# Performance work log

Hardware: AMD Instinct MI355X
Metric: run time of the kernel (lower is better)

The kernel has to match this reference:

```python
import jax, jax.numpy as jnp
import numpy as np

B, S, E = 2, 2048, 2048
H, KV, D = 16, 4, 128
G = H // KV
ROPE_THETA = 10000.0


def setup_inputs() -> dict:
    key = jax.random.key(0)
    ks = jax.random.split(key, 8)
    std = 0.02
    return {
        "x": jax.random.normal(ks[0], (B, S, E), jnp.float32),
        "Wq": jax.random.normal(ks[1], (H * D, E), jnp.float32) * std,
        "bq": jax.random.normal(ks[2], (H * D,), jnp.float32) * std,
        "Wk": jax.random.normal(ks[3], (KV * D, E), jnp.float32) * std,
        "bk": jax.random.normal(ks[4], (KV * D,), jnp.float32) * std,
        "Wv": jax.random.normal(ks[5], (KV * D, E), jnp.float32) * std,
        "bv": jax.random.normal(ks[6], (KV * D,), jnp.float32) * std,
        "Wo": jax.random.normal(ks[7], (E, H * D), jnp.float32) * std,
    }


def _rope_cos_sin(seq_len, head_dim):
    inv_freq = 1.0 / (ROPE_THETA ** (jnp.arange(0, head_dim, 2, dtype=jnp.float32) / head_dim))
    pos = jnp.arange(seq_len, dtype=jnp.float32)  # rope scale factor = 1.0
    freqs = pos[:, None] * inv_freq[None, :]        # [S, D/2]
    emb = jnp.concatenate([freqs, freqs], axis=-1)  # [S, D]
    return jnp.cos(emb), jnp.sin(emb)


def _apply_rope(t, cos, sin):
    # t: [..., S, <extra dims>, D]; cos/sin: [S, D] broadcast over extra dims
    half = t.shape[-1] // 2
    extra = t.ndim - 3  # dims between S (axis 1) and D (last)
    c = cos.reshape((1, cos.shape[0]) + (1,) * extra + (cos.shape[1],))
    s = sin.reshape((1, sin.shape[0]) + (1,) * extra + (sin.shape[1],))
    rot = jnp.concatenate([-t[..., half:], t[..., :half]], axis=-1)
    return t * c + rot * s


def reference(x, Wq, bq, Wk, bk, Wv, bv, Wo):
    b, s, e = x.shape
    # QKV projections (biases on q/k/v, none on o)
    q = (jnp.einsum("bse,he->bsh", x, Wq) + bq).reshape(b, s, KV, G, D)
    k = (jnp.einsum("bse,he->bsh", x, Wk) + bk).reshape(b, s, KV, D)
    v = (jnp.einsum("bse,he->bsh", x, Wv) + bv).reshape(b, s, KV, D)

    cos, sin = _rope_cos_sin(s, D)
    q = _apply_rope(q, cos, sin)
    k = _apply_rope(k, cos, sin)

    scale = 1.0 / jnp.sqrt(jnp.float32(D))
    # GQA: q heads grouped per kv head; k/v broadcast over group dim
    scores = jnp.einsum("bskgd,btkd->bkgst", q, k) * scale  # [B,KV,G,S,S]
    causal = jnp.tril(jnp.ones((s, s), dtype=bool))
    scores = jnp.where(causal, scores, jnp.float32(-1e9))
    attn = jax.nn.softmax(scores, axis=-1)
    out = jnp.einsum("bkgst,btkd->bskgd", attn, v).reshape(b, s, H * D)
    return jnp.einsum("bsh,eh->bse", out, Wo)
```

## Files before the change

### kernel.cpp

```cpp
#include <hip/hip_runtime.h>
#include <hip/hip_bf16.h>
#include <math.h>

#define BB 2
#define SS 2048
#define EE 2048
#define HH 16
#define KVH 4
#define DD 128
#define QTILES 32

typedef short short8 __attribute__((ext_vector_type(8)));
typedef float f32x4 __attribute__((ext_vector_type(4)));

__device__ __forceinline__ unsigned int f2bf1(float x) {
    union { float f; unsigned int u; } v; v.f = x;
    return (v.u + 0x7FFFu + ((v.u >> 16) & 1u)) >> 16;
}
__device__ __forceinline__ unsigned int packbf(float a, float b) {
    return f2bf1(a) | (f2bf1(b) << 16);
}
__device__ __forceinline__ float bf2f(unsigned short u) {
    union { unsigned int u; float f; } v; v.u = ((unsigned int)u) << 16;
    return v.f;
}
__device__ __forceinline__ void gl_lds16(const void* g, void* l) {
    __builtin_amdgcn_global_load_lds(
        (const __attribute__((address_space(1))) unsigned int*)g,
        (__attribute__((address_space(3))) unsigned int*)l,
        16, 0, 0);
}

__global__ __launch_bounds__(256) void cvt_bf16_kernel(
    const float* __restrict__ in, unsigned short* __restrict__ out, int n4)
{
    int i = blockIdx.x * 256 + threadIdx.x;
    if (i < n4) {
        float4 f = ((const float4*)in)[i];
        ((uint2*)out)[i] = make_uint2(packbf(f.x, f.y), packbf(f.z, f.w));
    }
}

__global__ __launch_bounds__(256) void concat_bias_kernel(
    const float* __restrict__ bk, const float* __restrict__ bv, float* __restrict__ bkv)
{
    int i = blockIdx.x * 256 + threadIdx.x;
    bkv[i] = (i < 512) ? bk[i] : bv[i - 512];
}

template <bool OUT_BF16>
__global__ __launch_bounds__(256) void gemm_mfma_kernel(
    const unsigned short* __restrict__ A, const unsigned short* __restrict__ W,
    const float* __restrict__ bias, void* __restrict__ Cout,
    int M, int N, int K)
{
    __shared__ unsigned short As[128 * 32];
    __shared__ unsigned short Bs[128 * 32];

    const int tid  = threadIdx.x;
    const int w    = tid >> 6;
    const int lane = tid & 63;
    const int quad = lane >> 4;
    const int l16  = lane & 15;
    const int wr   = w >> 1, wc = w & 1;
    const int m0 = blockIdx.y * 128, n0 = blockIdx.x * 128;

    f32x4 acc[4][4];
#pragma unroll
    for (int i = 0; i < 4; ++i)
#pragma unroll
        for (int j = 0; j < 4; ++j) acc[i][j] = (f32x4){0.f, 0.f, 0.f, 0.f};

    const unsigned short* Ag = A + (size_t)(m0 + w * 32 + (lane >> 2)) * K + (lane & 3) * 8;
    const unsigned short* Wg = W + (size_t)(n0 + w * 32 + (lane >> 2)) * K + (lane & 3) * 8;
    unsigned short* AsB = &As[(w * 32) * 32];
    unsigned short* BsB = &Bs[(w * 32) * 32];

    for (int k0 = 0; k0 < K; k0 += 32) {
        gl_lds16(Ag + k0, AsB);
        gl_lds16(Ag + k0 + (size_t)16 * K, AsB + 16 * 32);
        gl_lds16(Wg + k0, BsB);
        gl_lds16(Wg + k0 + (size_t)16 * K, BsB + 16 * 32);
        __syncthreads();

        short8 a_f[4], b_f[4];
#pragma unroll
        for (int i = 0; i < 4; ++i)
            a_f[i] = *(const short8*)&As[(wr * 64 + i * 16 + l16) * 32 + quad * 8];
#pragma unroll
        for (int j = 0; j < 4; ++j)
            b_f[j] = *(const short8*)&Bs[(wc * 64 + j * 16 + l16) * 32 + quad * 8];
#pragma unroll
        for (int i = 0; i < 4; ++i)
#pragma unroll
            for (int j = 0; j < 4; ++j)
                acc[i][j] = __builtin_amdgcn_mfma_f32_16x16x32_bf16(a_f[i], b_f[j], acc[i][j], 0, 0, 0);
        __syncthreads();
    }

    float bj[4];
#pragma unroll
    for (int j = 0; j < 4; ++j)
        bj[j] = bias ? bias[n0 + wc * 64 + j * 16 + l16] : 0.0f;
#pragma unroll
    for (int i = 0; i < 4; ++i) {
#pragma unroll
        for (int r = 0; r < 4; ++r) {
            size_t row = m0 + wr * 64 + i * 16 + quad * 4 + r;
#pragma unroll
            for (int j = 0; j < 4; ++j) {
                size_t col = n0 + wc * 64 + j * 16 + l16;
                float val = acc[i][j][r] + bj[j];
                if (OUT_BF16)
                    ((unsigned short*)Cout)[row * N + col] = (unsigned short)f2bf1(val);
                else
                    ((float*)Cout)[row * N + col] = val;
            }
        }
    }
}

__global__ __launch_bounds__(64) void rope_bf16_kernel(
    unsigned short* __restrict__ t, int nh, int rowstride)
{
    int m = blockIdx.x / nh;
    int h = blockIdx.x % nh;
    int s = m % SS;
    int d = threadIdx.x;
    unsigned short* p = t + (size_t)m * rowstride + h * 128;
    float inv_freq = expf(-(float)d * (logf(10000.0f) / 64.0f));
    float fr = (float)s * inv_freq;
    float c = cosf(fr), sn = sinf(fr);
    float x1 = bf2f(p[d]), x2 = bf2f(p[d + 64]);
    p[d]      = (unsigned short)f2bf1(x1 * c - x2 * sn);
    p[d + 64] = (unsigned short)f2bf1(x2 * c + x1 * sn);
}

__global__ __launch_bounds__(256, 2) void attn_mfma_kernel(
    const unsigned short* __restrict__ q, const unsigned short* __restrict__ kvb,
    unsigned short* __restrict__ o)
{
    __shared__ unsigned int Ks_u[64 * 68];
    __shared__ unsigned int Vs_u[128 * 36];
    __shared__ short Ps[4][16 * 72];

    const int tid  = threadIdx.x;
    const int w    = tid >> 6;
    const int lane = tid & 63;
    const int quad = lane >> 4;
    const int l16  = lane & 15;
    const int jpair = blockIdx.x;
    const int h     = blockIdx.y;
    const int b     = blockIdx.z;
    const int kv    = h >> 2;

    const float scale = 0.08838834764831845f;
    const unsigned short* kbase = kvb + (size_t)b * SS * 1024 + kv * 128;
    const unsigned short* vbase = kbase + 512;

    for (int pass = 0; pass < 2; ++pass) {
        const int qt = pass ? (QTILES - 1 - jpair) : jpair;
        const int q0 = qt * 64;

        short8 qf[4];
        {
            const int sq = q0 + w * 16 + l16;
            const unsigned short* qp = q + (size_t)(b * SS + sq) * 2048 + h * 128 + quad * 8;
#pragma unroll
            for (int ks = 0; ks < 4; ++ks)
                qf[ks] = *(const short8*)(qp + ks * 32);
        }

        float m_r[4], l_r[4];
        f32x4 Oacc[8];
#pragma unroll
        for (int r = 0; r < 4; ++r) { m_r[r] = -1e30f; l_r[r] = 0.0f; }
#pragma unroll
        for (int ot = 0; ot < 8; ++ot) Oacc[ot] = (f32x4){0.f, 0.f, 0.f, 0.f};

        for (int t = 0; t <= qt; ++t) {
            const int p0 = t * 64;

            {
                const int c  = tid & 15;
                const int pb = tid >> 4;
#pragma unroll
                for (int rr = 0; rr < 4; ++rr) {
                    int pos = pb + rr * 16;
                    *(uint4*)(&Ks_u[pos * 68 + c * 4]) =
                        *(const uint4*)(kbase + (size_t)(p0 + pos) * 1024 + c * 8);
                }
            }
            {
                const int pp   = tid >> 3;
                const int dseg = (tid & 7) * 16;
                const unsigned short* va = vbase + (size_t)(p0 + 2 * pp) * 1024 + dseg;
                uint4 ua0 = *(const uint4*)(va);
                uint4 ua1 = *(const uint4*)(va + 8);
                uint4 ub0 = *(const uint4*)(va + 1024);
                uint4 ub1 = *(const uint4*)(va + 1024 + 8);
#define WR2(i, a, bb2) { \
    Vs_u[(dseg + (i)) * 36 + pp]     = ((a) & 0xffffu) | ((bb2) << 16); \
    Vs_u[(dseg + (i) + 1) * 36 + pp] = ((a) >> 16) | ((bb2) & 0xffff0000u); }
                WR2(0,  ua0.x, ub0.x) WR2(2,  ua0.y, ub0.y)
                WR2(4,  ua0.z, ub0.z) WR2(6,  ua0.w, ub0.w)
                WR2(8,  ua1.x, ub1.x) WR2(10, ua1.y, ub1.y)
                WR2(12, ua1.z, ub1.z) WR2(14, ua1.w, ub1.w)
#undef WR2
            }
            __syncthreads();

            f32x4 S[4];
#pragma unroll
            for (int ct = 0; ct < 4; ++ct) {
                f32x4 s = (f32x4){0.f, 0.f, 0.f, 0.f};
#pragma unroll
                for (int ks = 0; ks < 4; ++ks) {
                    short8 kf = *(const short8*)(&Ks_u[(ct * 16 + l16) * 68 + ks * 16 + quad * 4]);
                    s = __builtin_amdgcn_mfma_f32_16x16x32_bf16(qf[ks], kf, s, 0, 0, 0);
                }
#pragma unroll
                for (int r = 0; r < 4; ++r) s[r] *= scale;
                S[ct] = s;
            }

            if (t == qt) {
                const int rowloc = w * 16 + quad * 4;
#pragma unroll
                for (int ct = 0; ct < 4; ++ct)
#pragma unroll
                    for (int r = 0; r < 4; ++r)
                        if (ct * 16 + l16 > rowloc + r) S[ct][r] = -1e30f;
            }

            float mnew[4];
#pragma unroll
            for (int r = 0; r < 4; ++r) {
                float c0 = fmaxf(fmaxf(S[0][r], S[1][r]), fmaxf(S[2][r], S[3][r]));
                c0 = fmaxf(c0, __shfl_xor(c0, 1));
                c0 = fmaxf(c0, __shfl_xor(c0, 2));
                c0 = fmaxf(c0, __shfl_xor(c0, 4));
                c0 = fmaxf(c0, __shfl_xor(c0, 8));
                mnew[r] = fmaxf(m_r[r], c0);
            }
#pragma unroll
            for (int r = 0; r < 4; ++r) {
                float alpha = __expf(m_r[r] - mnew[r]);
                m_r[r] = mnew[r];
                float rs = 0.0f;
#pragma unroll
                for (int ct = 0; ct < 4; ++ct) {
                    float p = __expf(S[ct][r] - mnew[r]);
                    rs += p;
                    Ps[w][(quad * 4 + r) * 72 + ct * 16 + l16] = (short)f2bf1(p);
                }
                rs += __shfl_xor(rs, 1);
                rs += __shfl_xor(rs, 2);
                rs += __shfl_xor(rs, 4);
                rs += __shfl_xor(rs, 8);
                l_r[r] = l_r[r] * alpha + rs;
#pragma unroll
                for (int ot = 0; ot < 8; ++ot) Oacc[ot][r] *= alpha;
            }

            short8 pf0 = *(const short8*)(&Ps[w][l16 * 72 + quad * 8]);
            short8 pf1 = *(const short8*)(&Ps[w][l16 * 72 + 32 + quad * 8]);
#pragma unroll
            for (int ot = 0; ot < 8; ++ot) {
                short8 b0 = *(const short8*)((const short*)&Vs_u[(ot * 16 + l16) * 36 + quad * 4]);
                Oacc[ot] = __builtin_amdgcn_mfma_f32_16x16x32_bf16(pf0, b0, Oacc[ot], 0, 0, 0);
                short8 b1 = *(const short8*)((const short*)&Vs_u[(ot * 16 + l16) * 36 + 16 + quad * 4]);
                Oacc[ot] = __builtin_amdgcn_mfma_f32_16x16x32_bf16(pf1, b1, Oacc[ot], 0, 0, 0);
            }
            __syncthreads();
        }

        float inv[4];
#pragma unroll
        for (int r = 0; r < 4; ++r) inv[r] = 1.0f / l_r[r];
        const int orow0 = q0 + w * 16 + quad * 4;
        unsigned short* ob = o + (size_t)(b * SS + orow0) * 2048 + h * 128 + l16;
#pragma unroll
        for (int r = 0; r < 4; ++r)
#pragma unroll
            for (int ot = 0; ot < 8; ++ot)
                ob[(size_t)r * 2048 + ot * 16] = (unsigned short)f2bf1(Oacc[ot][r] * inv[r]);
    }
}

extern "C" void kernel_launch(void* const* d_in, const int* in_sizes, int n_in,
                              void* d_out, int out_size, void* d_ws, size_t ws_size,
                              hipStream_t stream)
{
    const float* x  = (const float*)d_in[0];
    const float* Wq = (const float*)d_in[1];
    const float* bq = (const float*)d_in[2];
    const float* Wk = (const float*)d_in[3];
    const float* bk = (const float*)d_in[4];
    const float* Wv = (const float*)d_in[5];
    const float* bv = (const float*)d_in[6];
    const float* Wo = (const float*)d_in[7];
    float* out = (float*)d_out;

    const int M = BB * SS;
    char* wsb = (char*)d_ws;
    unsigned short* xb   = (unsigned short*)wsb;  wsb += (size_t)M * EE * 2;
    unsigned short* wqb  = (unsigned short*)wsb;  wsb += (size_t)EE * EE * 2;
    unsigned short* wkvb = (unsigned short*)wsb;  wsb += (size_t)1024 * EE * 2;
    unsigned short* wob  = (unsigned short*)wsb;  wsb += (size_t)EE * EE * 2;
    unsigned short* qb   = (unsigned short*)wsb;  wsb += (size_t)M * 2048 * 2;
    unsigned short* kvb  = (unsigned short*)wsb;  wsb += (size_t)M * 1024 * 2;
    unsigned short* abb  = (unsigned short*)wsb;  wsb += (size_t)M * 2048 * 2;
    float* bkv = (float*)wsb;

    cvt_bf16_kernel<<<(M * EE / 4) / 256, 256, 0, stream>>>(x, xb, M * EE / 4);
    cvt_bf16_kernel<<<(EE * EE / 4) / 256, 256, 0, stream>>>(Wq, wqb, EE * EE / 4);
    cvt_bf16_kernel<<<(512 * EE / 4) / 256, 256, 0, stream>>>(Wk, wkvb, 512 * EE / 4);
    cvt_bf16_kernel<<<(512 * EE / 4) / 256, 256, 0, stream>>>(Wv, wkvb + (size_t)512 * EE, 512 * EE / 4);
    cvt_bf16_kernel<<<(EE * EE / 4) / 256, 256, 0, stream>>>(Wo, wob, EE * EE / 4);
    concat_bias_kernel<<<4, 256, 0, stream>>>(bk, bv, bkv);

    gemm_mfma_kernel<true><<<dim3(2048 / 128, M / 128), 256, 0, stream>>>(
        xb, wqb, bq, qb, M, 2048, EE);
    gemm_mfma_kernel<true><<<dim3(1024 / 128, M / 128), 256, 0, stream>>>(
        xb, wkvb, bkv, kvb, M, 1024, EE);

    rope_bf16_kernel<<<M * HH, 64, 0, stream>>>(qb, HH, 2048);
    rope_bf16_kernel<<<M * KVH, 64, 0, stream>>>(kvb, KVH, 1024);

    attn_mfma_kernel<<<dim3(16, HH, BB), 256, 0, stream>>>(qb, kvb, abb);

    gemm_mfma_kernel<false><<<dim3(EE / 128, M / 128), 256, 0, stream>>>(
        abb, wob, nullptr, out, M, EE, 2048);
}
```

Measured before the change: 421.3 us.

## Fuse QKV projection, merge prep kernels, double-buffer and swizzle attention LDS

Merges all fp32-to-bf16 conversions and the bias concatenation into one launch, fuses the Q and KV projections into a single GEMM over a combined QKV buffer, and merges the two RoPE launches. In the attention kernel, K/V tiles are prefetched into registers and stored into double-buffered LDS with XOR swizzles instead of padding, which removes one barrier per tile. Softmax now uses exp2 with the scale folded in. This cuts launch overhead and LDS bank conflicts at the cost of more registers and more complex indexing.

```diff
diff --git a/kernel.cpp b/kernel.cpp
--- a/kernel.cpp
+++ b/kernel.cpp
@@ -20,10 +20,6 @@
 __device__ __forceinline__ unsigned int packbf(float a, float b) {
     return f2bf1(a) | (f2bf1(b) << 16);
 }
-__device__ __forceinline__ float bf2f(unsigned short u) {
-    union { unsigned int u; float f; } v; v.u = ((unsigned int)u) << 16;
-    return v.f;
-}
 __device__ __forceinline__ void gl_lds16(const void* g, void* l) {
     __builtin_amdgcn_global_load_lds(
         (const __attribute__((address_space(1))) unsigned int*)g,
@@ -31,21 +27,32 @@
         16, 0, 0);
 }
 
-__global__ __launch_bounds__(256) void cvt_bf16_kernel(
-    const float* __restrict__ in, unsigned short* __restrict__ out, int n4)
-{
-    int i = blockIdx.x * 256 + threadIdx.x;
-    if (i < n4) {
-        float4 f = ((const float4*)in)[i];
-        ((uint2*)out)[i] = make_uint2(packbf(f.x, f.y), packbf(f.z, f.w));
-    }
-}
-
-__global__ __launch_bounds__(256) void concat_bias_kernel(
-    const float* __restrict__ bk, const float* __restrict__ bv, float* __restrict__ bkv)
-{
-    int i = blockIdx.x * 256 + threadIdx.x;
-    bkv[i] = (i < 512) ? bk[i] : bv[i - 512];
+__global__ __launch_bounds__(256) void cvt_all_kernel(
+    const float* __restrict__ x,  const float* __restrict__ Wq,
+    const float* __restrict__ Wk, const float* __restrict__ Wv,
+    const float* __restrict__ Wo, const float* __restrict__ bq,
+    const float* __restrict__ bk, const float* __restrict__ bv,
+    unsigned short* __restrict__ xb, unsigned short* __restrict__ wqkv,
+    unsigned short* __restrict__ wob, float* __restrict__ bqkv)
+{
+    long id = (long)blockIdx.x * 256 + threadIdx.x;
+    const float* src; unsigned short* dst; long j;
+    if (id < 2097152)      { j = id;           src = x;  dst = xb; }
+    else if (id < 3145728) { j = id - 2097152; src = Wq; dst = wqkv; }
+    else if (id < 3407872) { j = id - 3145728; src = Wk; dst = wqkv + 4194304; }
+    else if (id < 3670016) { j = id - 3407872; src = Wv; dst = wqkv + 5242880; }
+    else if (id < 4718592) { j = id - 3670016; src = Wo; dst = wob; }
+    else if (id < 4719360) {
+        long c = (id - 4718592) * 4;
+#pragma unroll
+        for (int e = 0; e < 4; ++e) {
+            long cc = c + e;
+            bqkv[cc] = (cc < 2048) ? bq[cc] : (cc < 2560 ? bk[cc - 2048] : bv[cc - 2560]);
+        }
+        return;
+    } else return;
+    float4 f = ((const float4*)src)[j];
+    ((uint2*)dst)[j] = make_uint2(packbf(f.x, f.y), packbf(f.z, f.w));
 }
 
 template <bool OUT_BF16>
@@ -120,29 +127,31 @@
     }
 }
 
-__global__ __launch_bounds__(64) void rope_bf16_kernel(
-    unsigned short* __restrict__ t, int nh, int rowstride)
-{
-    int m = blockIdx.x / nh;
-    int h = blockIdx.x % nh;
-    int s = m % SS;
+__global__ __launch_bounds__(64) void rope_kernel(unsigned short* __restrict__ qkv)
+{
+    int bix = blockIdx.x;
+    int m, col;
+    if (bix < 65536) { m = bix >> 4; col = (bix & 15) * 128; }
+    else { int i = bix - 65536; m = i >> 2; col = 2048 + (i & 3) * 128; }
+    int s = m & (SS - 1);
     int d = threadIdx.x;
-    unsigned short* p = t + (size_t)m * rowstride + h * 128;
+    unsigned short* p = qkv + (size_t)m * 3072 + col;
     float inv_freq = expf(-(float)d * (logf(10000.0f) / 64.0f));
     float fr = (float)s * inv_freq;
     float c = cosf(fr), sn = sinf(fr);
-    float x1 = bf2f(p[d]), x2 = bf2f(p[d + 64]);
-    p[d]      = (unsigned short)f2bf1(x1 * c - x2 * sn);
-    p[d + 64] = (unsigned short)f2bf1(x2 * c + x1 * sn);
+    union { unsigned int u; float f; } x1, x2;
+    x1.u = ((unsigned int)p[d]) << 16;
+    x2.u = ((unsigned int)p[d + 64]) << 16;
+    p[d]      = (unsigned short)f2bf1(x1.f * c - x2.f * sn);
+    p[d + 64] = (unsigned short)f2bf1(x2.f * c + x1.f * sn);
 }
 
 __global__ __launch_bounds__(256, 2) void attn_mfma_kernel(
-    const unsigned short* __restrict__ q, const unsigned short* __restrict__ kvb,
-    unsigned short* __restrict__ o)
-{
-    __shared__ unsigned int Ks_u[64 * 68];
-    __shared__ unsigned int Vs_u[128 * 36];
-    __shared__ short Ps[4][16 * 72];
+    const unsigned short* __restrict__ qkv, unsigned short* __restrict__ o)
+{
+    __shared__ unsigned int Ks_u[2][64 * 64];
+    __shared__ unsigned int Vs_u[2][128 * 32];
+    __shared__ unsigned short Ps[4][16 * 64];
 
     const int tid  = threadIdx.x;
     const int w    = tid >> 6;
@@ -154,9 +163,15 @@
     const int b     = blockIdx.z;
     const int kv    = h >> 2;
 
-    const float scale = 0.08838834764831845f;
-    const unsigned short* kbase = kvb + (size_t)b * SS * 1024 + kv * 128;
+    const float k2 = 0.12752789744920764f;
+
+    const unsigned short* kbase = qkv + (size_t)b * SS * 3072 + 2048 + kv * 128;
     const unsigned short* vbase = kbase + 512;
+
+    const int kc  = tid & 15;
+    const int kp0 = tid >> 4;
+    const int vpp = tid >> 3;
+    const int vd0 = (tid & 7) * 16;
 
     for (int pass = 0; pass < 2; ++pass) {
         const int qt = pass ? (QTILES - 1 - jpair) : jpair;
@@ -164,13 +179,25 @@
 
         short8 qf[4];
         {
-            const int sq = q0 + w * 16 + l16;
-            const unsigned short* qp = q + (size_t)(b * SS + sq) * 2048 + h * 128 + quad * 8;
+            const unsigned short* qp = qkv + (size_t)(b * SS + q0 + w * 16 + l16) * 3072 + h * 128 + quad * 8;
 #pragma unroll
             for (int ks = 0; ks < 4; ++ks)
                 qf[ks] = *(const short8*)(qp + ks * 32);
         }
 
+        uint4 kpre[4], vpa[2], vpb[2];
+        {
+            const unsigned short* kg = kbase + (size_t)kp0 * 3072 + kc * 8;
+#pragma unroll
+            for (int rr = 0; rr < 4; ++rr)
+                kpre[rr] = *(const uint4*)(kg + (size_t)rr * 16 * 3072);
+            const unsigned short* vg = vbase + (size_t)(2 * vpp) * 3072 + vd0;
+            vpa[0] = *(const uint4*)(vg);
+            vpa[1] = *(const uint4*)(vg + 8);
+            vpb[0] = *(const uint4*)(vg + 3072);
+            vpb[1] = *(const uint4*)(vg + 3072 + 8);
+        }
+
         float m_r[4], l_r[4];
         f32x4 Oacc[8];
 #pragma unroll
@@ -179,34 +206,42 @@
         for (int ot = 0; ot < 8; ++ot) Oacc[ot] = (f32x4){0.f, 0.f, 0.f, 0.f};
 
         for (int t = 0; t <= qt; ++t) {
-            const int p0 = t * 64;
-
+            const int buf = t & 1;
+            unsigned int* Kb = Ks_u[buf];
+            unsigned int* Vb = Vs_u[buf];
+
+#pragma unroll
+            for (int rr = 0; rr < 4; ++rr) {
+                int pos = kp0 + rr * 16;
+                int key = (kp0 + rr) & 7;
+                *(uint4*)&Kb[pos * 64 + (kc ^ key) * 4] = kpre[rr];
+            }
             {
-                const int c  = tid & 15;
-                const int pb = tid >> 4;
-#pragma unroll
-                for (int rr = 0; rr < 4; ++rr) {
-                    int pos = pb + rr * 16;
-                    *(uint4*)(&Ks_u[pos * 68 + c * 4]) =
-                        *(const uint4*)(kbase + (size_t)(p0 + pos) * 1024 + c * 8);
+                const unsigned int* pa = (const unsigned int*)vpa;
+                const unsigned int* pb = (const unsigned int*)vpb;
+#pragma unroll
+                for (int j = 0; j < 8; ++j) {
+                    unsigned lo = __builtin_amdgcn_perm(pb[j], pa[j], 0x05040100);
+                    unsigned hi = __builtin_amdgcn_perm(pb[j], pa[j], 0x07060302);
+                    int d0 = vd0 + 2 * j;
+                    int g  = d0 >> 4;
+                    int k0 = (d0 + g) & 7;
+                    int k1 = (d0 + 1 + g) & 7;
+                    Vb[d0 * 32 + (((vpp >> 2) ^ k0) & 7) * 4 + (vpp & 3)] = lo;
+                    Vb[(d0 + 1) * 32 + (((vpp >> 2) ^ k1) & 7) * 4 + (vpp & 3)] = hi;
                 }
             }
-            {
-                const int pp   = tid >> 3;
-                const int dseg = (tid & 7) * 16;
-                const unsigned short* va = vbase + (size_t)(p0 + 2 * pp) * 1024 + dseg;
-                uint4 ua0 = *(const uint4*)(va);
-                uint4 ua1 = *(const uint4*)(va + 8);
-                uint4 ub0 = *(const uint4*)(va + 1024);
-                uint4 ub1 = *(const uint4*)(va + 1024 + 8);
-#define WR2(i, a, bb2) { \
-    Vs_u[(dseg + (i)) * 36 + pp]     = ((a) & 0xffffu) | ((bb2) << 16); \
-    Vs_u[(dseg + (i) + 1) * 36 + pp] = ((a) >> 16) | ((bb2) & 0xffff0000u); }
-                WR2(0,  ua0.x, ub0.x) WR2(2,  ua0.y, ub0.y)
-                WR2(4,  ua0.z, ub0.z) WR2(6,  ua0.w, ub0.w)
-                WR2(8,  ua1.x, ub1.x) WR2(10, ua1.y, ub1.y)
-                WR2(12, ua1.z, ub1.z) WR2(14, ua1.w, ub1.w)
-#undef WR2
+
+            if (t < qt) {
+                const unsigned short* kg = kbase + (size_t)((t + 1) * 64 + kp0) * 3072 + kc * 8;
+#pragma unroll
+                for (int rr = 0; rr < 4; ++rr)
+                    kpre[rr] = *(const uint4*)(kg + (size_t)rr * 16 * 3072);
+                const unsigned short* vg = vbase + (size_t)((t + 1) * 64 + 2 * vpp) * 3072 + vd0;
+                vpa[0] = *(const uint4*)(vg);
+                vpa[1] = *(const uint4*)(vg + 8);
+                vpb[0] = *(const uint4*)(vg + 3072);
+                vpb[1] = *(const uint4*)(vg + 3072 + 8);
             }
             __syncthreads();
 
@@ -214,13 +249,13 @@
 #pragma unroll
             for (int ct = 0; ct < 4; ++ct) {
                 f32x4 s = (f32x4){0.f, 0.f, 0.f, 0.f};
+                const int row = ct * 16 + l16;
+                const int key = (l16 + ct) & 7;
 #pragma unroll
                 for (int ks = 0; ks < 4; ++ks) {
-                    short8 kf = *(const short8*)(&Ks_u[(ct * 16 + l16) * 68 + ks * 16 + quad * 4]);
+                    short8 kf = *(const short8*)&Kb[row * 64 + ((ks * 4 + quad) ^ key) * 4];
                     s = __builtin_amdgcn_mfma_f32_16x16x32_bf16(qf[ks], kf, s, 0, 0, 0);
                 }
-#pragma unroll
-                for (int r = 0; r < 4; ++r) s[r] *= scale;
                 S[ct] = s;
             }
 
@@ -233,7 +268,6 @@
                         if (ct * 16 + l16 > rowloc + r) S[ct][r] = -1e30f;
             }
 
-            float mnew[4];
 #pragma unroll
             for (int r = 0; r < 4; ++r) {
                 float c0 = fmaxf(fmaxf(S[0][r], S[1][r]), fmaxf(S[2][r], S[3][r]));
@@ -241,18 +275,21 @@
                 c0 = fmaxf(c0, __shfl_xor(c0, 2));
                 c0 = fmaxf(c0, __shfl_xor(c0, 4));
                 c0 = fmaxf(c0, __shfl_xor(c0, 8));
-                mnew[r] = fmaxf(m_r[r], c0);
-            }
-#pragma unroll
-            for (int r = 0; r < 4; ++r) {
-                float alpha = __expf(m_r[r] - mnew[r]);
-                m_r[r] = mnew[r];
+                float mnew = fmaxf(m_r[r], c0);
+                float alpha = exp2f((m_r[r] - mnew) * k2);
+                m_r[r] = mnew;
+                float mh = mnew * k2;
                 float rs = 0.0f;
+                const int prow = quad * 4 + r;
+                const int pkey = (prow >> 2) ^ ((prow & 3) << 1);
 #pragma unroll
                 for (int ct = 0; ct < 4; ++ct) {
-                    float p = __expf(S[ct][r] - mnew[r]);
+                    float p = exp2f(S[ct][r] * k2 - mh);
                     rs += p;
-                    Ps[w][(quad * 4 + r) * 72 + ct * 16 + l16] = (short)f2bf1(p);
+                    int chunk = ct * 2 + (l16 >> 3);
+                    union { float f; unsigned u; } pu; pu.f = p;
+                    Ps[w][prow * 64 + (chunk ^ pkey) * 8 + (l16 & 7)] =
+                        (unsigned short)((pu.u + 0x8000u) >> 16);
                 }
                 rs += __shfl_xor(rs, 1);
                 rs += __shfl_xor(rs, 2);
@@ -263,16 +300,20 @@
                 for (int ot = 0; ot < 8; ++ot) Oacc[ot][r] *= alpha;
             }
 
-            short8 pf0 = *(const short8*)(&Ps[w][l16 * 72 + quad * 8]);
-            short8 pf1 = *(const short8*)(&Ps[w][l16 * 72 + 32 + quad * 8]);
-#pragma unroll
-            for (int ot = 0; ot < 8; ++ot) {
-                short8 b0 = *(const short8*)((const short*)&Vs_u[(ot * 16 + l16) * 36 + quad * 4]);
-                Oacc[ot] = __builtin_amdgcn_mfma_f32_16x16x32_bf16(pf0, b0, Oacc[ot], 0, 0, 0);
-                short8 b1 = *(const short8*)((const short*)&Vs_u[(ot * 16 + l16) * 36 + 16 + quad * 4]);
-                Oacc[ot] = __builtin_amdgcn_mfma_f32_16x16x32_bf16(pf1, b1, Oacc[ot], 0, 0, 0);
-            }
-            __syncthreads();
+            {
+                const int pkeyr = (l16 >> 2) ^ ((l16 & 3) << 1);
+                short8 pf0 = *(const short8*)&Ps[w][l16 * 64 + (quad ^ pkeyr) * 8];
+                short8 pf1 = *(const short8*)&Ps[w][l16 * 64 + ((4 + quad) ^ pkeyr) * 8];
+#pragma unroll
+                for (int ot = 0; ot < 8; ++ot) {
+                    const int d = ot * 16 + l16;
+                    const int vkey = (l16 + ot) & 7;
+                    short8 v0 = *(const short8*)&Vb[d * 32 + (quad ^ vkey) * 4];
+                    Oacc[ot] = __builtin_amdgcn_mfma_f32_16x16x32_bf16(pf0, v0, Oacc[ot], 0, 0, 0);
+                    short8 v1 = *(const short8*)&Vb[d * 32 + ((4 + quad) ^ vkey) * 4];
+                    Oacc[ot] = __builtin_amdgcn_mfma_f32_16x16x32_bf16(pf1, v1, Oacc[ot], 0, 0, 0);
+                }
+            }
         }
 
         float inv[4];
@@ -285,6 +326,8 @@
 #pragma unroll
             for (int ot = 0; ot < 8; ++ot)
                 ob[(size_t)r * 2048 + ot * 16] = (unsigned short)f2bf1(Oacc[ot][r] * inv[r]);
+
+        __syncthreads();
     }
 }
 
@@ -305,30 +348,21 @@
     const int M = BB * SS;
     char* wsb = (char*)d_ws;
     unsigned short* xb   = (unsigned short*)wsb;  wsb += (size_t)M * EE * 2;
-    unsigned short* wqb  = (unsigned short*)wsb;  wsb += (size_t)EE * EE * 2;
-    unsigned short* wkvb = (unsigned short*)wsb;  wsb += (size_t)1024 * EE * 2;
+    unsigned short* wqkv = (unsigned short*)wsb;  wsb += (size_t)3072 * EE * 2;
     unsigned short* wob  = (unsigned short*)wsb;  wsb += (size_t)EE * EE * 2;
-    unsigned short* qb   = (unsigned short*)wsb;  wsb += (size_t)M * 2048 * 2;
-    unsigned short* kvb  = (unsigned short*)wsb;  wsb += (size_t)M * 1024 * 2;
+    unsigned short* qkvb = (unsigned short*)wsb;  wsb += (size_t)M * 3072 * 2;
     unsigned short* abb  = (unsigned short*)wsb;  wsb += (size_t)M * 2048 * 2;
-    float* bkv = (float*)wsb;
-
-    cvt_bf16_kernel<<<(M * EE / 4) / 256, 256, 0, stream>>>(x, xb, M * EE / 4);
-    cvt_bf16_kernel<<<(EE * EE / 4) / 256, 256, 0, stream>>>(Wq, wqb, EE * EE / 4);
-    cvt_bf16_kernel<<<(512 * EE / 4) / 256, 256, 0, stream>>>(Wk, wkvb, 512 * EE / 4);
-    cvt_bf16_kernel<<<(512 * EE / 4) / 256, 256, 0, stream>>>(Wv, wkvb + (size_t)512 * EE, 512 * EE / 4);
-    cvt_bf16_kernel<<<(EE * EE / 4) / 256, 256, 0, stream>>>(Wo, wob, EE * EE / 4);
-    concat_bias_kernel<<<4, 256, 0, stream>>>(bk, bv, bkv);
-
-    gemm_mfma_kernel<true><<<dim3(2048 / 128, M / 128), 256, 0, stream>>>(
-        xb, wqb, bq, qb, M, 2048, EE);
-    gemm_mfma_kernel<true><<<dim3(1024 / 128, M / 128), 256, 0, stream>>>(
-        xb, wkvb, bkv, kvb, M, 1024, EE);
-
-    rope_bf16_kernel<<<M * HH, 64, 0, stream>>>(qb, HH, 2048);
-    rope_bf16_kernel<<<M * KVH, 64, 0, stream>>>(kvb, KVH, 1024);
-
-    attn_mfma_kernel<<<dim3(16, HH, BB), 256, 0, stream>>>(qb, kvb, abb);
+    float* bqkv = (float*)wsb;
+
+    cvt_all_kernel<<<18435, 256, 0, stream>>>(x, Wq, Wk, Wv, Wo, bq, bk, bv,
+                                              xb, wqkv, wob, bqkv);
+
+    gemm_mfma_kernel<true><<<dim3(3072 / 128, M / 128), 256, 0, stream>>>(
+        xb, wqkv, bqkv, qkvb, M, 3072, EE);
+
+    rope_kernel<<<M * HH + M * KVH, 64, 0, stream>>>(qkvb);
+
+    attn_mfma_kernel<<<dim3(16, HH, BB), 256, 0, stream>>>(qkvb, abb);
 
     gemm_mfma_kernel<false><<<dim3(EE / 128, M / 128), 256, 0, stream>>>(
         abb, wob, nullptr, out, M, EE, 2048);
```

Measured after the change: 376.3 us. 10.7% less time.
